# Kernel tuning notes

Hardware: AMD Instinct MI355X
Metric: run time of the kernel (lower is better)

The kernel has to match this reference:

```python
import jax, jax.numpy as jnp
import numpy as np

B, NVEC, DIM, HEADS, DH, M, ITERS, DEPTH, NCLASS, KER = 8, 4096, 512, 8, 64, 256, 6, 2, 10, 33
INNER = HEADS * DH


def _ln(x, g, b, eps=1e-5):
    mu = x.mean(-1, keepdims=True)
    var = ((x - mu) ** 2).mean(-1, keepdims=True)
    return (x - mu) * jax.lax.rsqrt(var + eps) * g + b


def _mp_pinv(x, iters=ITERS):
    # Moore-Penrose pseudo-inverse via Newton-Schulz iterations (lucidrains).
    # x: [b, h, m, m]
    abs_x = jnp.abs(x)
    col = abs_x.sum(-1).max(-1)  # [b, h]
    row = abs_x.sum(-2).max(-1)  # [b, h]
    z = jnp.swapaxes(x, -1, -2) / (col * row)[..., None, None]
    I = jnp.eye(x.shape[-1], dtype=x.dtype)
    for _ in range(iters):
        xz = x @ z
        z = 0.25 * z @ (13.0 * I - xz @ (15.0 * I - xz @ (7.0 * I - xz)))
    return z


def _nystrom_attn(x, qkv_w, out_w, out_b, conv_w):
    b, n, _ = x.shape
    qkv = x @ qkv_w  # [b, n, 3*inner]
    q, k, v = jnp.split(qkv, 3, axis=-1)
    to_h = lambda t: t.reshape(b, n, HEADS, DH).transpose(0, 2, 1, 3)  # [b,h,n,dh]
    q, k, v = to_h(q), to_h(k), to_h(v)
    q = q * (DH ** -0.5)

    l = n // M  # tokens per landmark segment (n divisible by M)
    q_l = q.reshape(b, HEADS, M, l, DH).mean(3)  # [b,h,M,dh]
    k_l = k.reshape(b, HEADS, M, l, DH).mean(3)

    attn1 = jax.nn.softmax(jnp.einsum('bhnd,bhmd->bhnm', q, k_l), axis=-1)    # [b,h,n,M]
    attn2 = jax.nn.softmax(jnp.einsum('bhmd,bhld->bhml', q_l, k_l), axis=-1)  # [b,h,M,M]
    attn3 = jax.nn.softmax(jnp.einsum('bhmd,bhnd->bhmn', q_l, k), axis=-1)    # [b,h,M,n]

    out = (attn1 @ _mp_pinv(attn2)) @ (attn3 @ v)  # [b,h,n,dh]

    # residual depthwise conv over sequence dim (kernel 33, groups=heads, no bias)
    out = out + jax.lax.conv_general_dilated(
        v, conv_w, (1, 1), [(KER // 2, KER // 2), (0, 0)],
        dimension_numbers=('NCHW', 'OIHW', 'NCHW'), feature_group_count=HEADS)

    out = out.transpose(0, 2, 1, 3).reshape(b, n, INNER)
    return out @ out_w + out_b


def setup_inputs():
    key = jax.random.key(0)
    ks = jax.random.split(key, 12)
    s = 0.02
    f32 = jnp.float32
    return {
        'x': jax.random.normal(ks[0], (B, NVEC, 2), f32),
        'lin_w': jax.random.normal(ks[1], (2, DIM), f32) * s,
        'lin_b': jnp.zeros((DIM,), f32),
        'ln1_g': jnp.ones((DEPTH, DIM), f32),
        'ln1_b': jnp.zeros((DEPTH, DIM), f32),
        'qkv_w': jax.random.normal(ks[2], (DEPTH, DIM, 3 * INNER), f32) * s,
        'out_w': jax.random.normal(ks[3], (DEPTH, INNER, DIM), f32) * s,
        'out_b': jnp.zeros((DEPTH, DIM), f32),
        'conv_w': jax.random.normal(ks[4], (DEPTH, HEADS, 1, KER, 1), f32) * s,
        'ln2_g': jnp.ones((DEPTH, DIM), f32),
        'ln2_b': jnp.zeros((DEPTH, DIM), f32),
        'ff1_w': jax.random.normal(ks[5], (DEPTH, DIM, 4 * DIM), f32) * s,
        'ff1_b': jnp.zeros((DEPTH, 4 * DIM), f32),
        'ff2_w': jax.random.normal(ks[6], (DEPTH, 4 * DIM, DIM), f32) * s,
        'ff2_b': jnp.zeros((DEPTH, DIM), f32),
        'final_w': jax.random.normal(ks[7], (NVEC * DIM, NCLASS), f32) * s,
        'final_b': jnp.zeros((NCLASS,), f32),
    }


def reference(x, lin_w, lin_b, ln1_g, ln1_b, qkv_w, out_w, out_b, conv_w,
              ln2_g, ln2_b, ff1_w, ff1_b, ff2_w, ff2_b, final_w, final_b):
    h = x @ lin_w + lin_b  # [B, NVEC, DIM]
    for i in range(DEPTH):
        h = h + _nystrom_attn(_ln(h, ln1_g[i], ln1_b[i]), qkv_w[i], out_w[i], out_b[i], conv_w[i])
        z = _ln(h, ln2_g[i], ln2_b[i])
        h = h + (jax.nn.gelu(z @ ff1_w[i] + ff1_b[i]) @ ff2_w[i] + ff2_b[i])
    return h.reshape(h.shape[0], -1) @ final_w + final_b  # [B, NCLASS]
```

## Files before the change

kernel.cpp:

```cpp
#include <hip/hip_runtime.h>
#include <hip/hip_bf16.h>

#define BB_ 8
#define NVEC 4096
#define DIM 512
#define HEADS 8
#define DH 64
#define MM_ 256
#define ITERS 6
#define DEPTH 2
#define NCLASS 10
#define KER 33
#define INNER 512
#define LSEG 16

typedef long long ll;
typedef __bf16 bh16;
typedef __attribute__((ext_vector_type(8))) __bf16 bf16x8;
typedef __attribute__((ext_vector_type(4))) float f32x4;

template<int WR, int WC, bool TRB, bool GELU_ACT, bool RESID, bool BF16OUT, bool DUAL>
__global__ void __launch_bounds__(256)
mgemm_k(const bh16* __restrict__ A, const bh16* __restrict__ B,
        const float* __restrict__ bias, void* __restrict__ Cv, void* __restrict__ C2v,
        int K, int lda, int ldb, int ldc,
        int BI, ll sAo, ll sAi, ll sBo, ll sBi, ll sCo, ll sCi,
        float alpha, float diagv)
{
    constexpr int BM = WR * 64, BN = WC * 64;
    const int bz = blockIdx.z;
    const int bo = bz / BI, bi = bz % BI;
    const bh16* Ab = A + bo * sAo + (ll)bi * sAi;
    const bh16* Bb = B + bo * sBo + (ll)bi * sBi;
    const ll coff = bo * sCo + (ll)bi * sCi;
    const int m0 = blockIdx.y * BM;
    const int n0 = blockIdx.x * BN;
    const int tid = threadIdx.x;
    const int lane = tid & 63;
    const int wave = tid >> 6;
    const int wr = wave / WC, wc = wave % WC;

    __shared__ bh16 Al[BM * 32];
    __shared__ bh16 Bl[BN * 32];

    f32x4 acc[4][4];
#pragma unroll
    for (int i = 0; i < 4; ++i)
#pragma unroll
        for (int j = 0; j < 4; ++j) acc[i][j] = (f32x4){0.f, 0.f, 0.f, 0.f};

    const int srow = tid >> 2;
    const int ssl  = tid & 3;

    const int rsel  = ((lane & 15) >> 1) & 3;
    const int kslot = lane >> 4;

    for (int k0 = 0; k0 < K; k0 += 32) {
        __syncthreads();
#pragma unroll
        for (int i = 0; i < BM / 64; ++i) {
            int row = i * 64 + srow;
            int gsl = ssl ^ ((row >> 1) & 3);
            __builtin_amdgcn_global_load_lds(
                (const __attribute__((address_space(1))) unsigned int*)
                    (Ab + (ll)(m0 + row) * lda + k0 + gsl * 8),
                (__attribute__((address_space(3))) unsigned int*)
                    (Al + row * 32 + ssl * 8),
                16, 0, 0);
        }
        if (!TRB) {
#pragma unroll
            for (int i = 0; i < BN / 64; ++i) {
                int row = i * 64 + srow;
                int gsl = ssl ^ ((row >> 1) & 3);
                __builtin_amdgcn_global_load_lds(
                    (const __attribute__((address_space(1))) unsigned int*)
                        (Bb + (ll)(n0 + row) * ldb + k0 + gsl * 8),
                    (__attribute__((address_space(3))) unsigned int*)
                        (Bl + row * 32 + ssl * 8),
                    16, 0, 0);
            }
        } else {
            const int bk = tid >> 3;
            const int nb0 = (tid & 7) * (BN / 8);
#pragma unroll
            for (int v8 = 0; v8 < BN / 64; ++v8) {
                int nb = nb0 + v8 * 8;
                bf16x8 v = *(const bf16x8*)(Bb + (ll)(k0 + bk) * ldb + n0 + nb);
#pragma unroll
                for (int j = 0; j < 8; ++j) {
                    int n = nb + j;
                    int sl = (bk >> 3) ^ ((n >> 1) & 3);
                    Bl[n * 32 + sl * 8 + (bk & 7)] = v[j];
                }
            }
        }
        __syncthreads();

        bf16x8 af[4], bfr[4];
#pragma unroll
        for (int mi = 0; mi < 4; ++mi) {
            int row = wr * 64 + mi * 16 + (lane & 15);
            af[mi] = *(const bf16x8*)(Al + row * 32 + (kslot ^ rsel) * 8);
        }
#pragma unroll
        for (int ni = 0; ni < 4; ++ni) {
            int row = wc * 64 + ni * 16 + (lane & 15);
            bfr[ni] = *(const bf16x8*)(Bl + row * 32 + (kslot ^ rsel) * 8);
        }
#pragma unroll
        for (int mi = 0; mi < 4; ++mi)
#pragma unroll
            for (int ni = 0; ni < 4; ++ni)
                acc[mi][ni] = __builtin_amdgcn_mfma_f32_16x16x32_bf16(
                    af[mi], bfr[ni], acc[mi][ni], 0, 0, 0);
    }

#pragma unroll
    for (int mi = 0; mi < 4; ++mi) {
#pragma unroll
        for (int ni = 0; ni < 4; ++ni) {
            const int colg = n0 + wc * 64 + ni * 16 + (lane & 15);
            const float bia = (!DUAL && bias) ? bias[colg] : 0.f;
#pragma unroll
            for (int r = 0; r < 4; ++r) {
                const int rowg = m0 + wr * 64 + mi * 16 + (lane >> 4) * 4 + r;
                const float a = acc[mi][ni][r];
                const ll off = coff + (ll)rowg * ldc + colg;
                if (DUAL) {
                    ((bh16*)Cv)[off] = (bh16)a;
                    float w = ((rowg == colg) ? diagv : 0.f) - a;
                    ((bh16*)C2v)[off] = (bh16)w;
                } else {
                    float v = alpha * a + bia;
                    if (diagv != 0.f && rowg == colg) v += diagv;
                    if (GELU_ACT) {
                        float t = tanhf(0.7978845608f * (v + 0.044715f * v * v * v));
                        v = 0.5f * v * (1.0f + t);
                    }
                    if (BF16OUT) {
                        ((bh16*)Cv)[off] = (bh16)v;
                    } else {
                        float* p = (float*)Cv + off;
                        float o = v;
                        if (RESID) o += *p;
                        *p = o;
                    }
                }
            }
        }
    }
}

template<int WR, int WC, bool TRB, bool G, bool R, bool BO, bool D>
static inline void mg(hipStream_t s, int M, int N, int K,
                      const bh16* A, int lda, const bh16* B, int ldb,
                      void* C, int ldc, void* C2, const float* bias,
                      int batch, int BI,
                      ll sAo, ll sAi, ll sBo, ll sBi, ll sCo, ll sCi,
                      float alpha, float diagv)
{
    dim3 grid(N / (WC * 64), M / (WR * 64), batch);
    hipLaunchKernelGGL((mgemm_k<WR, WC, TRB, G, R, BO, D>), grid, dim3(256), 0, s,
                       A, B, bias, C, C2, K, lda, ldb, ldc, BI,
                       sAo, sAi, sBo, sBi, sCo, sCi, alpha, diagv);
}

__global__ void embed_k(const float* __restrict__ x, const float* __restrict__ w,
                        const float* __restrict__ b, float* __restrict__ h)
{
    ll idx = (ll)blockIdx.x * 256 + threadIdx.x;
    int d = (int)(idx & 511);
    ll bn = idx >> 9;
    h[idx] = x[bn * 2] * w[d] + x[bn * 2 + 1] * w[512 + d] + b[d];
}

__global__ void __launch_bounds__(256)
ln_k(const float* __restrict__ X, const float* __restrict__ g,
     const float* __restrict__ bta, bh16* __restrict__ Y)
{
    const ll row = blockIdx.x;
    const float* x = X + row * 512;
    bh16* y = Y + row * 512;
    const int tid = threadIdx.x;
    float v0 = x[tid], v1 = x[tid + 256];
    float s = v0 + v1;
    float q = v0 * v0 + v1 * v1;
    __shared__ float sred[8];
    for (int o = 32; o; o >>= 1) { s += __shfl_down(s, o); q += __shfl_down(q, o); }
    const int lane = tid & 63, w = tid >> 6;
    if (lane == 0) { sred[w] = s; sred[4 + w] = q; }
    __syncthreads();
    float ssum = sred[0] + sred[1] + sred[2] + sred[3];
    float qsum = sred[4] + sred[5] + sred[6] + sred[7];
    float mu = ssum * (1.0f / 512.0f);
    float var = qsum * (1.0f / 512.0f) - mu * mu;
    float r = rsqrtf(var + 1e-5f);
    y[tid] = (bh16)((v0 - mu) * r * g[tid] + bta[tid]);
    y[tid + 256] = (bh16)((v1 - mu) * r * g[tid + 256] + bta[tid + 256]);
}

__global__ void __launch_bounds__(256)
cvtT_k(const float* __restrict__ in, bh16* __restrict__ outp, int C, int R)
{
    __shared__ float t[64][65];
    const int nCt = C >> 6;
    const int c0 = (blockIdx.x % nCt) * 64;
    const int r0 = (blockIdx.x / nCt) * 64;
    const int tid = threadIdx.x;
#pragma unroll
    for (int j = 0; j < 16; ++j) {
        int idx = j * 256 + tid;
        int lr = idx >> 6, lc = idx & 63;
        t[lc][lr] = in[(ll)(r0 + lr) * C + c0 + lc];
    }
    __syncthreads();
#pragma unroll
    for (int v = 0; v < 2; ++v) {
        int flat = v * 256 + tid;
        int lc = flat >> 3, r8 = (flat & 7) * 8;
        bf16x8 o;
#pragma unroll
        for (int j = 0; j < 8; ++j) o[j] = (bh16)t[lc][r8 + j];
        *(bf16x8*)(outp + (ll)(c0 + lc) * R + r0 + r8) = o;
    }
}

__global__ void landmarks_k(const bh16* __restrict__ qkv,
                            bh16* __restrict__ qlb, bh16* __restrict__ klb)
{
    int idx = blockIdx.x * 256 + threadIdx.x;
    int d = idx & 63;
    int m = (idx >> 6) & 255;
    int h = (idx >> 14) & 7;
    int b = idx >> 17;
    const bh16* base = qkv + (ll)b * (NVEC * 1536) + (ll)(m * LSEG) * 1536 + h * 64 + d;
    float sq = 0.f, sk = 0.f;
#pragma unroll
    for (int l = 0; l < LSEG; ++l) {
        sq += (float)base[(ll)l * 1536];
        sk += (float)base[(ll)l * 1536 + 512];
    }
    ll o = (ll)(b * 8 + h) * 16384 + m * 64 + d;
    qlb[o] = (bh16)(sq * (0.0625f * 0.125f));
    klb[o] = (bh16)(sk * 0.0625f);
}

__global__ void wbt_k(const bh16* __restrict__ wb, bh16* __restrict__ wbt)
{
    int idx = blockIdx.x * 256 + threadIdx.x;
    int d = idx & 63, kg = (idx >> 6) & 31, bhh = idx >> 11;
    const bh16* p = wb + (ll)bhh * 16384 + kg * 8 * 64 + d;
    bf16x8 o;
#pragma unroll
    for (int j = 0; j < 8; ++j) o[j] = p[j * 64];
    *(bf16x8*)(wbt + (ll)bhh * 16384 + d * 256 + kg * 8) = o;
}

__global__ void a3vred_k(const float* __restrict__ part, bh16* __restrict__ outp)
{
    int idx = blockIdx.x * 256 + threadIdx.x;
    int smp = idx >> 17;
    int rest = idx & 131071;
    int h = rest >> 14, o = rest & 16383;
    const float* p = part + (ll)smp * 1048576 + (ll)h * 131072 + o;
    float s = 0.f;
#pragma unroll
    for (int j = 0; j < 8; ++j) s += p[j * 16384];
    outp[(ll)(smp * 8 + h) * 16384 + o] = (bh16)s;
}

__global__ void __launch_bounds__(256)
conv_k(const bh16* __restrict__ qkv, const float* __restrict__ cw,
       bh16* __restrict__ convo)
{
    int idx = blockIdx.x * 256 + threadIdx.x;
    int c8 = idx & 63;
    int ng = (idx >> 6) & 1023;
    int b  = idx >> 16;
    const int n0 = ng * 4;
    const int h = c8 >> 3;
    const bh16* v = qkv + (ll)b * (NVEC * 1536) + 1024 + c8 * 8;

    float wreg[KER];
#pragma unroll
    for (int k = 0; k < KER; ++k) wreg[k] = cw[h * KER + k];

    float acc[4][8];
#pragma unroll
    for (int t = 0; t < 4; ++t)
#pragma unroll
        for (int e = 0; e < 8; ++e) acc[t][e] = 0.f;

#pragma unroll
    for (int m = 0; m < 36; ++m) {
        int nn = n0 + m - (KER / 2);
        bf16x8 vv = {};
        if ((unsigned)nn < (unsigned)NVEC)
            vv = *(const bf16x8*)(v + (ll)nn * 1536);
#pragma unroll
        for (int t = 0; t < 4; ++t) {
            constexpr int KMAX = KER - 1;
            int k = m - t;
            if (k >= 0 && k <= KMAX) {
                float wk = wreg[k];
#pragma unroll
                for (int e = 0; e < 8; ++e)
                    acc[t][e] = fmaf((float)vv[e], wk, acc[t][e]);
            }
        }
    }

    bh16* o = convo + (ll)b * (NVEC * 512) + (ll)n0 * 512 + c8 * 8;
#pragma unroll
    for (int t = 0; t < 4; ++t) {
        bf16x8 ov;
#pragma unroll
        for (int e = 0; e < 8; ++e) ov[e] = (bh16)acc[t][e];
        *(bf16x8*)(o + (ll)t * 512) = ov;
    }
}

__device__ __forceinline__ float blkmax(float m, float* red, int tid)
{
#pragma unroll
    for (int o = 32; o; o >>= 1) m = fmaxf(m, __shfl_down(m, o));
    if ((tid & 63) == 0) red[tid >> 6] = m;
    __syncthreads();
    m = fmaxf(fmaxf(red[0], red[1]), fmaxf(red[2], red[3]));
    __syncthreads();
    return m;
}
__device__ __forceinline__ float blksum(float s, float* red, int tid)
{
#pragma unroll
    for (int o = 32; o; o >>= 1) s += __shfl_down(s, o);
    if ((tid & 63) == 0) red[tid >> 6] = s;
    __syncthreads();
    s = red[0] + red[1] + red[2] + red[3];
    __syncthreads();
    return s;
}

__global__ void __launch_bounds__(256)
softmax_bf_k(bh16* __restrict__ X, int L)
{
    const ll row = blockIdx.x;
    bh16* x = X + row * (ll)L;
    const int tid = threadIdx.x;
    __shared__ float red[4];
    float v[16];
    bf16x8 a = *(const bf16x8*)(x + tid * 8);
    bf16x8 b = *(const bf16x8*)(x + 2048 + tid * 8);
#pragma unroll
    for (int j = 0; j < 8; ++j) { v[j] = (float)a[j]; v[8 + j] = (float)b[j]; }
    float m = -1e30f;
#pragma unroll
    for (int j = 0; j < 16; ++j) m = fmaxf(m, v[j]);
    m = blkmax(m, red, tid);
    float s = 0.f;
#pragma unroll
    for (int j = 0; j < 16; ++j) { v[j] = __expf(v[j] - m); s += v[j]; }
    s = blksum(s, red, tid);
    float inv = 1.0f / s;
    bf16x8 oa, ob;
#pragma unroll
    for (int j = 0; j < 8; ++j) { oa[j] = (bh16)(v[j] * inv); ob[j] = (bh16)(v[8 + j] * inv); }
    *(bf16x8*)(x + tid * 8) = oa;
    *(bf16x8*)(x + 2048 + tid * 8) = ob;
}

__global__ void __launch_bounds__(256)
softmax256_k(bh16* __restrict__ X)
{
    const int tid = threadIdx.x;
    const ll row = (ll)blockIdx.x * 8 + (tid >> 5);
    const int l = tid & 31;
    bh16* x = X + row * 256 + l * 8;
    bf16x8 a = *(const bf16x8*)x;
    float v[8];
#pragma unroll
    for (int j = 0; j < 8; ++j) v[j] = (float)a[j];
    float m = -1e30f;
#pragma unroll
    for (int j = 0; j < 8; ++j) m = fmaxf(m, v[j]);
#pragma unroll
    for (int o = 16; o; o >>= 1) m = fmaxf(m, __shfl_xor(m, o, 32));
    float s = 0.f;
#pragma unroll
    for (int j = 0; j < 8; ++j) { v[j] = __expf(v[j] - m); s += v[j]; }
#pragma unroll
    for (int o = 16; o; o >>= 1) s += __shfl_xor(s, o, 32);
    float inv = 1.0f / s;
    bf16x8 ov;
#pragma unroll
    for (int j = 0; j < 8; ++j) ov[j] = (bh16)(v[j] * inv);
    *(bf16x8*)x = ov;
}

__global__ void __launch_bounds__(256)
pinv_init_k(const bh16* __restrict__ X, bh16* __restrict__ Z)
{
    const ll bh = blockIdx.x;
    const bh16* x = X + bh * 65536;
    bh16* z = Z + bh * 65536;
    const int tid = threadIdx.x;
    float rs = 0.f, cs = 0.f;
    for (int j = 0; j < 256; ++j) {
        rs += fabsf((float)x[tid * 256 + j]);
        cs += fabsf((float)x[j * 256 + tid]);
    }
    __shared__ float rbuf[256], cbuf[256];
    rbuf[tid] = rs; cbuf[tid] = cs;
    __syncthreads();
    for (int o = 128; o; o >>= 1) {
        if (tid < o) {
            rbuf[tid] = fmaxf(rbuf[tid], rbuf[tid + o]);
            cbuf[tid] = fmaxf(cbuf[tid], cbuf[tid + o]);
        }
        __syncthreads();
    }
    float inv = 1.0f / (rbuf[0] * cbuf[0]);
    for (int e = tid; e < 65536; e += 256) {
        int i = e >> 8, j = e & 255;
        z[e] = (bh16)((float)x[j * 256 + i] * inv);
    }
}

__global__ void final_init_k(const float* __restrict__ fb, float* __restrict__ out)
{
    int i = threadIdx.x;
    if (i < BB_ * NCLASS) out[i] = fb[i % NCLASS];
}

__global__ void __launch_bounds__(256)
final_gemv_k(const float* __restrict__ hbuf, const float* __restrict__ w,
             float* __restrict__ out)
{
    const int half = blockIdx.y;
    const int chunk = blockIdx.x;
    const int tid = threadIdx.x;
    const int k0 = chunk * 8192;
    float pc[4][NCLASS] = {};
    for (int e = 0; e < 32; ++e) {
        int k = k0 + e * 256 + tid;
        const float* wr = w + (ll)k * NCLASS;
        float wv[NCLASS];
#pragma unroll
        for (int c = 0; c < NCLASS; ++c) wv[c] = wr[c];
#pragma unroll
        for (int b = 0; b < 4; ++b) {
            float hv = hbuf[(ll)(half * 4 + b) * (NVEC * DIM) + k];
#pragma unroll
            for (int c = 0; c < NCLASS; ++c) pc[b][c] = fmaf(hv, wv[c], pc[b][c]);
        }
    }
    __shared__ float red[4][4][NCLASS];
    const int lane = tid & 63, wv_ = tid >> 6;
#pragma unroll
    for (int b = 0; b < 4; ++b)
#pragma unroll
        for (int c = 0; c < NCLASS; ++c) {
            float s = pc[b][c];
#pragma unroll
            for (int o = 32; o; o >>= 1) s += __shfl_down(s, o);
            if (lane == 0) red[wv_][b][c] = s;
        }
    __syncthreads();
    if (tid < 4 * NCLASS) {
        int b = tid / NCLASS, c = tid % NCLASS;
        float s = red[0][b][c] + red[1][b][c] + red[2][b][c] + red[3][b][c];
        atomicAdd(out + (half * 4 + b) * NCLASS + c, s);
    }
}

extern "C" void kernel_launch(void* const* d_in, const int* in_sizes, int n_in,
                              void* d_out, int out_size, void* d_ws, size_t ws_size,
                              hipStream_t stream)
{
    const float* x      = (const float*)d_in[0];
    const float* lin_w  = (const float*)d_in[1];
    const float* lin_b  = (const float*)d_in[2];
    const float* ln1_g  = (const float*)d_in[3];
    const float* ln1_b  = (const float*)d_in[4];
    const float* qkv_w  = (const float*)d_in[5];
    const float* out_w  = (const float*)d_in[6];
    const float* out_b  = (const float*)d_in[7];
    const float* conv_w = (const float*)d_in[8];
    const float* ln2_g  = (const float*)d_in[9];
    const float* ln2_b  = (const float*)d_in[10];
    const float* ff1_w  = (const float*)d_in[11];
    const float* ff1_b  = (const float*)d_in[12];
    const float* ff2_w  = (const float*)d_in[13];
    const float* ff2_b  = (const float*)d_in[14];
    const float* final_w = (const float*)d_in[15];
    const float* final_b = (const float*)d_in[16];
    float* out = (float*)d_out;
    float* ws  = (float*)d_ws;

    float* H    = ws;
    bh16*  QKV  = (bh16*)(ws + 16777216);
    float* P    = ws + 41943040;
    bh16*  qlbf = (bh16*)(ws + 52428800);
    bh16*  klbf = (bh16*)(ws + 52953088);
    bh16*  A3Vb = (bh16*)(ws + 53477376);
    bh16*  WBb  = (bh16*)(ws + 54001664);
    bh16*  WBT  = (bh16*)(ws + 54525952);
    bh16*  WQT  = (bh16*)(ws + 55050240);
    bh16*  WOT  = (bh16*)(ws + 55443456);
    bh16*  F1WT = (bh16*)(ws + 55574528);
    bh16*  F2WT = (bh16*)(ws + 56098816);
    if (ws_size < 56623104ULL * 4) return;

    bh16*  XLNall = (bh16*)P;
    bh16*  ATT3c  = (bh16*)P;
    float* A3Vp   = P + 8388608;
    bh16*  CONVa  = (bh16*)P;
    bh16*  Xbf = (bh16*)P;
    bh16*  Z0  = (bh16*)(P + 2097152);
    bh16*  Z1  = (bh16*)(P + 4194304);
    bh16*  T1  = (bh16*)(P + 6291456);
    bh16*  T2  = (bh16*)(P + 8388608);
    bh16*  ATT1c  = (bh16*)P;
    bh16*  AOUTc  = (bh16*)(P + 8388608);
    bh16*  XLNc   = (bh16*)P;
    bh16*  HIDc   = (bh16*)(P + 2097152);

    const ll SMP = (ll)NVEC * 1536;

    hipLaunchKernelGGL(embed_k, dim3(65536), dim3(256), 0, stream, x, lin_w, lin_b, H);

    for (int i = 0; i < DEPTH; ++i) {
        const float* wq  = qkv_w + (ll)i * 512 * 1536;
        const float* wo  = out_w + (ll)i * 512 * 512;
        const float* bo  = out_b + (ll)i * 512;
        const float* cw  = conv_w + (ll)i * HEADS * KER;
        const float* g1  = ln1_g + (ll)i * 512;
        const float* b1  = ln1_b + (ll)i * 512;
        const float* g2  = ln2_g + (ll)i * 512;
        const float* b2  = ln2_b + (ll)i * 512;
        const float* f1w = ff1_w + (ll)i * 512 * 2048;
        const float* f1b = ff1_b + (ll)i * 2048;
        const float* f2w = ff2_w + (ll)i * 2048 * 512;
        const float* f2b = ff2_b + (ll)i * 512;

        hipLaunchKernelGGL(cvtT_k, dim3(192), dim3(256), 0, stream, wq, WQT, 1536, 512);
        hipLaunchKernelGGL(cvtT_k, dim3(64), dim3(256), 0, stream, wo, WOT, 512, 512);
        hipLaunchKernelGGL(cvtT_k, dim3(256), dim3(256), 0, stream, f1w, F1WT, 2048, 512);
        hipLaunchKernelGGL(cvtT_k, dim3(256), dim3(256), 0, stream, f2w, F2WT, 512, 2048);

        hipLaunchKernelGGL(ln_k, dim3(32768), dim3(256), 0, stream, H, g1, b1, XLNall);
        mg<2,2,0,0,0,1,0>(stream, 32768, 1536, 512, XLNall, 512, WQT, 512,
            QKV, 1536, nullptr, nullptr, 1, 1, 0,0, 0,0, 0,0, 1.f, 0.f);

        hipLaunchKernelGGL(landmarks_k, dim3(4096), dim3(256), 0, stream, QKV, qlbf, klbf);

        for (int c = 0; c < 4; ++c) {
            const bh16* qkvc = QKV + (ll)c * 2 * SMP;
            mg<2,2,0,0,0,1,0>(stream, 256, 4096, 64,
                qlbf + (ll)c * 262144, 64, qkvc + 512, 1536,
                ATT3c, 4096, nullptr, nullptr, 16, 8,
                131072, 16384, SMP, 64, 8388608LL, 1048576, 1.f, 0.f);
            hipLaunchKernelGGL(softmax_bf_k, dim3(4096), dim3(256), 0, stream, ATT3c, 4096);
            for (int s = 0; s < 2; ++s) {
                mg<4,1,1,0,0,0,0>(stream, 256, 64, 512,
                    ATT3c + (ll)s * 8 * 1048576, 4096, qkvc + (ll)s * SMP + 1024, 1536,
                    A3Vp + (ll)s * 1048576, 64, nullptr, nullptr, 64, 8,
                    1048576, 512, 64, 512LL * 1536, 131072, 16384, 1.f, 0.f);
            }
            hipLaunchKernelGGL(a3vred_k, dim3(1024), dim3(256), 0, stream,
                               A3Vp, A3Vb + (ll)c * 2 * 131072);
        }

        hipLaunchKernelGGL(conv_k, dim3(2048), dim3(256), 0, stream, QKV, cw, CONVa);
        mg<2,2,0,0,1,0,0>(stream, 32768, 512, 512, CONVa, 512, WOT, 512,
            H, 512, nullptr, nullptr, 1, 1, 0,0, 0,0, 0,0, 1.f, 0.f);

        mg<2,2,0,0,0,1,0>(stream, 256, 256, 64, qlbf, 64, klbf, 64,
            Xbf, 256, nullptr, nullptr, 64, 64, 0, 16384, 0, 16384, 0, 65536, 1.f, 0.f);
        hipLaunchKernelGGL(softmax256_k, dim3(2048), dim3(256), 0, stream, Xbf);
        hipLaunchKernelGGL(pinv_init_k, dim3(64), dim3(256), 0, stream, Xbf, Z0);
        bh16* zc = Z0; bh16* zn = Z1;
        for (int it = 0; it < ITERS; ++it) {
            mg<2,2,1,0,0,1,1>(stream, 256, 256, 256, Xbf, 256, zc, 256,
                T1, 256, T2, nullptr, 64, 64, 0, 65536, 0, 65536, 0, 65536, 1.f, 7.f);
            mg<2,2,1,0,0,1,0>(stream, 256, 256, 256, T1, 256, T2, 256,
                zn, 256, nullptr, nullptr, 64, 64, 0, 65536, 0, 65536, 0, 65536, -1.f, 15.f);
            mg<2,2,1,0,0,1,0>(stream, 256, 256, 256, T1, 256, zn, 256,
                T2, 256, nullptr, nullptr, 64, 64, 0, 65536, 0, 65536, 0, 65536, -1.f, 13.f);
            mg<2,2,1,0,0,1,0>(stream, 256, 256, 256, zc, 256, T2, 256,
                zn, 256, nullptr, nullptr, 64, 64, 0, 65536, 0, 65536, 0, 65536, 0.25f, 0.f);
            bh16* t = zc; zc = zn; zn = t;
        }
        mg<4,1,1,0,0,1,0>(stream, 256, 64, 256, zc, 256, A3Vb, 64,
            WBb, 64, nullptr, nullptr, 64, 64, 0, 65536, 0, 16384, 0, 16384, 1.f, 0.f);
        hipLaunchKernelGGL(wbt_k, dim3(512), dim3(256), 0, stream, WBb, WBT);

        for (int c = 0; c < 4; ++c) {
            const bh16* qkvc = QKV + (ll)c * 2 * SMP;
            mg<2,2,0,0,0,1,0>(stream, 4096, 256, 64,
                qkvc, 1536, klbf + (ll)c * 262144, 64,
                ATT1c, 256, nullptr, nullptr, 16, 8,
                SMP, 64, 131072, 16384, 8388608LL, 1048576, 0.125f, 0.f);
            hipLaunchKernelGGL(softmax256_k, dim3(8192), dim3(256), 0, stream, ATT1c);
            mg<4,1,0,0,0,1,0>(stream, 4096, 64, 256,
                ATT1c, 256, WBT + (ll)c * 262144, 256,
                AOUTc, 512, nullptr, nullptr, 16, 8,
                8388608LL, 1048576, 131072, 16384, 2097152LL, 64, 1.f, 0.f);
            mg<2,2,0,0,1,0,0>(stream, 8192, 512, 512, AOUTc, 512, WOT, 512,
                H + (ll)c * 2 * 2097152, 512, nullptr, bo, 1, 1, 0,0, 0,0, 0,0, 1.f, 0.f);
        }

        for (int c = 0; c < 4; ++c) {
            float* Hc = H + (ll)c * 2 * 2097152;
            hipLaunchKernelGGL(ln_k, dim3(8192), dim3(256), 0, stream, Hc, g2, b2, XLNc);
            mg<2,2,0,1,0,1,0>(stream, 8192, 2048, 512, XLNc, 512, F1WT, 512,
                HIDc, 2048, nullptr, f1b, 1, 1, 0,0, 0,0, 0,0, 1.f, 0.f);
            mg<2,2,0,0,1,0,0>(stream, 8192, 512, 2048, HIDc, 2048, F2WT, 2048,
                Hc, 512, nullptr, f2b, 1, 1, 0,0, 0,0, 0,0, 1.f, 0.f);
        }
    }

    hipLaunchKernelGGL(final_init_k, dim3(1), dim3(128), 0, stream, final_b, out);
    hipLaunchKernelGGL(final_gemv_k, dim3(256, 2), dim3(256), 0, stream, H, final_w, out);
}
```

Baseline: 3.526 ms.

## Fuse softmax into GEMM epilogue, fold conv into attention output, remap XCDs

Adds an SMAX epilogue to the GEMM that does a row softmax across the 256-wide tile, using shuffles and LDS for the cross-wave reduction. The separate softmax256 passes over attn1 and attn2 are removed. The depthwise conv output is now written in place over the k slice of QKV and added in the attn1·W GEMM epilogue (ADDC), which drops the extra full out-projection GEMM over the conv output. Workgroups are also remapped so that consecutive tiles land on the same XCD, aiming for better L2 locality. The trade-offs are more registers and syncs in the softmax path and overwriting k, which must no longer be needed by that point.

```diff
diff --git a/kernel.cpp b/kernel.cpp
--- a/kernel.cpp
+++ b/kernel.cpp
@@ -19,12 +19,14 @@
 typedef __attribute__((ext_vector_type(8))) __bf16 bf16x8;
 typedef __attribute__((ext_vector_type(4))) float f32x4;
 
-template<int WR, int WC, bool TRB, bool GELU_ACT, bool RESID, bool BF16OUT, bool DUAL>
+template<int WR, int WC, bool TRB, bool GELU_ACT, bool RESID, bool BF16OUT,
+         bool DUAL, bool SMAX, bool ADDC>
 __global__ void __launch_bounds__(256)
 mgemm_k(const bh16* __restrict__ A, const bh16* __restrict__ B,
         const float* __restrict__ bias, void* __restrict__ Cv, void* __restrict__ C2v,
         int K, int lda, int ldb, int ldc,
         int BI, ll sAo, ll sAi, ll sBo, ll sBi, ll sCo, ll sCi,
+        int ldc2, ll sC2o, ll sC2i,
         float alpha, float diagv)
 {
     constexpr int BM = WR * 64, BN = WC * 64;
@@ -33,8 +35,18 @@
     const bh16* Ab = A + bo * sAo + (ll)bi * sAi;
     const bh16* Bb = B + bo * sBo + (ll)bi * sBi;
     const ll coff = bo * sCo + (ll)bi * sCi;
-    const int m0 = blockIdx.y * BM;
-    const int n0 = blockIdx.x * BN;
+
+    const int gx = gridDim.x;
+    const int nwg = gx * gridDim.y;
+    int flat = blockIdx.y * gx + blockIdx.x;
+    {
+        int xcd = flat & 7, base = flat >> 3;
+        int q = nwg >> 3, rr = nwg & 7;
+        flat = (xcd < rr ? xcd * (q + 1) : rr * (q + 1) + (xcd - rr) * q) + base;
+    }
+    const int m0 = (flat / gx) * BM;
+    const int n0 = (flat % gx) * BN;
+
     const int tid = threadIdx.x;
     const int lane = tid & 63;
     const int wave = tid >> 6;
@@ -42,6 +54,7 @@
 
     __shared__ bh16 Al[BM * 32];
     __shared__ bh16 Bl[BN * 32];
+    __shared__ float srow[SMAX ? 4 * 64 : 4];
 
     f32x4 acc[4][4];
 #pragma unroll
@@ -49,8 +62,8 @@
 #pragma unroll
         for (int j = 0; j < 4; ++j) acc[i][j] = (f32x4){0.f, 0.f, 0.f, 0.f};
 
-    const int srow = tid >> 2;
-    const int ssl  = tid & 3;
+    const int srowi = tid >> 2;
+    const int ssl   = tid & 3;
 
     const int rsel  = ((lane & 15) >> 1) & 3;
     const int kslot = lane >> 4;
@@ -59,7 +72,7 @@
         __syncthreads();
 #pragma unroll
         for (int i = 0; i < BM / 64; ++i) {
-            int row = i * 64 + srow;
+            int row = i * 64 + srowi;
             int gsl = ssl ^ ((row >> 1) & 3);
             __builtin_amdgcn_global_load_lds(
                 (const __attribute__((address_space(1))) unsigned int*)
@@ -71,7 +84,7 @@
         if (!TRB) {
 #pragma unroll
             for (int i = 0; i < BN / 64; ++i) {
-                int row = i * 64 + srow;
+                int row = i * 64 + srowi;
                 int gsl = ssl ^ ((row >> 1) & 3);
                 __builtin_amdgcn_global_load_lds(
                     (const __attribute__((address_space(1))) unsigned int*)
@@ -116,6 +129,88 @@
                     af[mi], bfr[ni], acc[mi][ni], 0, 0, 0);
     }
 
+    if (SMAX) {
+        bh16* Cb = (bh16*)Cv;
+#pragma unroll
+        for (int mi = 0; mi < 4; ++mi)
+#pragma unroll
+            for (int ni = 0; ni < 4; ++ni)
+#pragma unroll
+                for (int r = 0; r < 4; ++r) acc[mi][ni][r] *= alpha;
+        float mx[4][4];
+#pragma unroll
+        for (int mi = 0; mi < 4; ++mi)
+#pragma unroll
+            for (int r = 0; r < 4; ++r) {
+                float m_ = acc[mi][0][r];
+#pragma unroll
+                for (int ni = 1; ni < 4; ++ni) m_ = fmaxf(m_, acc[mi][ni][r]);
+#pragma unroll
+                for (int msk = 1; msk < 16; msk <<= 1)
+                    m_ = fmaxf(m_, __shfl_xor(m_, msk));
+                mx[mi][r] = m_;
+            }
+        if ((lane & 15) == 0) {
+#pragma unroll
+            for (int mi = 0; mi < 4; ++mi)
+#pragma unroll
+                for (int r = 0; r < 4; ++r)
+                    srow[wc * 64 + mi * 16 + (lane >> 4) * 4 + r] = mx[mi][r];
+        }
+        __syncthreads();
+        float M_[4][4];
+#pragma unroll
+        for (int mi = 0; mi < 4; ++mi)
+#pragma unroll
+            for (int r = 0; r < 4; ++r) {
+                int row = mi * 16 + (lane >> 4) * 4 + r;
+                M_[mi][r] = fmaxf(fmaxf(srow[row], srow[64 + row]),
+                                  fmaxf(srow[128 + row], srow[192 + row]));
+            }
+        __syncthreads();
+        float sm[4][4];
+#pragma unroll
+        for (int mi = 0; mi < 4; ++mi)
+#pragma unroll
+            for (int r = 0; r < 4; ++r) {
+                float s_ = 0.f;
+#pragma unroll
+                for (int ni = 0; ni < 4; ++ni) {
+                    float e = __expf(acc[mi][ni][r] - M_[mi][r]);
+                    acc[mi][ni][r] = e;
+                    s_ += e;
+                }
+#pragma unroll
+                for (int msk = 1; msk < 16; msk <<= 1)
+                    s_ += __shfl_xor(s_, msk);
+                sm[mi][r] = s_;
+            }
+        if ((lane & 15) == 0) {
+#pragma unroll
+            for (int mi = 0; mi < 4; ++mi)
+#pragma unroll
+                for (int r = 0; r < 4; ++r)
+                    srow[wc * 64 + mi * 16 + (lane >> 4) * 4 + r] = sm[mi][r];
+        }
+        __syncthreads();
+#pragma unroll
+        for (int mi = 0; mi < 4; ++mi)
+#pragma unroll
+            for (int r = 0; r < 4; ++r) {
+                int row = mi * 16 + (lane >> 4) * 4 + r;
+                float inv = 1.0f / (srow[row] + srow[64 + row] +
+                                    srow[128 + row] + srow[192 + row]);
+                int rowg = m0 + row;
+#pragma unroll
+                for (int ni = 0; ni < 4; ++ni) {
+                    int colg = n0 + wc * 64 + ni * 16 + (lane & 15);
+                    Cb[coff + (ll)rowg * ldc + colg] = (bh16)(acc[mi][ni][r] * inv);
+                }
+            }
+        return;
+    }
+
+    const ll c2off = ADDC ? (bo * sC2o + (ll)bi * sC2i) : 0;
 #pragma unroll
     for (int mi = 0; mi < 4; ++mi) {
 #pragma unroll
@@ -133,6 +228,8 @@
                     ((bh16*)C2v)[off] = (bh16)w;
                 } else {
                     float v = alpha * a + bia;
+                    if (ADDC)
+                        v += (float)((const bh16*)C2v)[c2off + (ll)rowg * ldc2 + colg];
                     if (diagv != 0.f && rowg == colg) v += diagv;
                     if (GELU_ACT) {
                         float t = tanhf(0.7978845608f * (v + 0.044715f * v * v * v));
@@ -152,18 +249,19 @@
     }
 }
 
-template<int WR, int WC, bool TRB, bool G, bool R, bool BO, bool D>
+template<int WR, int WC, bool TRB, bool G, bool R, bool BO, bool D, bool SX, bool AC>
 static inline void mg(hipStream_t s, int M, int N, int K,
                       const bh16* A, int lda, const bh16* B, int ldb,
                       void* C, int ldc, void* C2, const float* bias,
                       int batch, int BI,
                       ll sAo, ll sAi, ll sBo, ll sBi, ll sCo, ll sCi,
-                      float alpha, float diagv)
+                      float alpha, float diagv,
+                      int ldc2 = 0, ll sC2o = 0, ll sC2i = 0)
 {
     dim3 grid(N / (WC * 64), M / (WR * 64), batch);
-    hipLaunchKernelGGL((mgemm_k<WR, WC, TRB, G, R, BO, D>), grid, dim3(256), 0, s,
+    hipLaunchKernelGGL((mgemm_k<WR, WC, TRB, G, R, BO, D, SX, AC>), grid, dim3(256), 0, s,
                        A, B, bias, C, C2, K, lda, ldb, ldc, BI,
-                       sAo, sAi, sBo, sBi, sCo, sCi, alpha, diagv);
+                       sAo, sAi, sBo, sBi, sCo, sCi, ldc2, sC2o, sC2i, alpha, diagv);
 }
 
 __global__ void embed_k(const float* __restrict__ x, const float* __restrict__ w,
@@ -271,8 +369,7 @@
 }
 
 __global__ void __launch_bounds__(256)
-conv_k(const bh16* __restrict__ qkv, const float* __restrict__ cw,
-       bh16* __restrict__ convo)
+conv_k(bh16* __restrict__ qkv, const float* __restrict__ cw)
 {
     int idx = blockIdx.x * 256 + threadIdx.x;
     int c8 = idx & 63;
@@ -311,13 +408,13 @@
         }
     }
 
-    bh16* o = convo + (ll)b * (NVEC * 512) + (ll)n0 * 512 + c8 * 8;
+    bh16* o = qkv + (ll)b * (NVEC * 1536) + (ll)n0 * 1536 + 512 + c8 * 8;
 #pragma unroll
     for (int t = 0; t < 4; ++t) {
         bf16x8 ov;
 #pragma unroll
         for (int e = 0; e < 8; ++e) ov[e] = (bh16)acc[t][e];
-        *(bf16x8*)(o + (ll)t * 512) = ov;
+        *(bf16x8*)(o + (ll)t * 1536) = ov;
     }
 }
 
@@ -368,34 +465,6 @@
     for (int j = 0; j < 8; ++j) { oa[j] = (bh16)(v[j] * inv); ob[j] = (bh16)(v[8 + j] * inv); }
     *(bf16x8*)(x + tid * 8) = oa;
     *(bf16x8*)(x + 2048 + tid * 8) = ob;
-}
-
-__global__ void __launch_bounds__(256)
-softmax256_k(bh16* __restrict__ X)
-{
-    const int tid = threadIdx.x;
-    const ll row = (ll)blockIdx.x * 8 + (tid >> 5);
-    const int l = tid & 31;
-    bh16* x = X + row * 256 + l * 8;
-    bf16x8 a = *(const bf16x8*)x;
-    float v[8];
-#pragma unroll
-    for (int j = 0; j < 8; ++j) v[j] = (float)a[j];
-    float m = -1e30f;
-#pragma unroll
-    for (int j = 0; j < 8; ++j) m = fmaxf(m, v[j]);
-#pragma unroll
-    for (int o = 16; o; o >>= 1) m = fmaxf(m, __shfl_xor(m, o, 32));
-    float s = 0.f;
-#pragma unroll
-    for (int j = 0; j < 8; ++j) { v[j] = __expf(v[j] - m); s += v[j]; }
-#pragma unroll
-    for (int o = 16; o; o >>= 1) s += __shfl_xor(s, o, 32);
-    float inv = 1.0f / s;
-    bf16x8 ov;
-#pragma unroll
-    for (int j = 0; j < 8; ++j) ov[j] = (bh16)(v[j] * inv);
-    *(bf16x8*)x = ov;
 }
 
 __global__ void __launch_bounds__(256)
@@ -515,7 +584,6 @@
     bh16*  XLNall = (bh16*)P;
     bh16*  ATT3c  = (bh16*)P;
     float* A3Vp   = P + 8388608;
-    bh16*  CONVa  = (bh16*)P;
     bh16*  Xbf = (bh16*)P;
     bh16*  Z0  = (bh16*)(P + 2097152);
     bh16*  Z1  = (bh16*)(P + 4194304);
@@ -550,20 +618,20 @@
         hipLaunchKernelGGL(cvtT_k, dim3(256), dim3(256), 0, stream, f2w, F2WT, 512, 2048);
 
         hipLaunchKernelGGL(ln_k, dim3(32768), dim3(256), 0, stream, H, g1, b1, XLNall);
-        mg<2,2,0,0,0,1,0>(stream, 32768, 1536, 512, XLNall, 512, WQT, 512,
+        mg<2,2,0,0,0,1,0,0,0>(stream, 32768, 1536, 512, XLNall, 512, WQT, 512,
             QKV, 1536, nullptr, nullptr, 1, 1, 0,0, 0,0, 0,0, 1.f, 0.f);
 
         hipLaunchKernelGGL(landmarks_k, dim3(4096), dim3(256), 0, stream, QKV, qlbf, klbf);
 
         for (int c = 0; c < 4; ++c) {
             const bh16* qkvc = QKV + (ll)c * 2 * SMP;
-            mg<2,2,0,0,0,1,0>(stream, 256, 4096, 64,
+            mg<2,2,0,0,0,1,0,0,0>(stream, 256, 4096, 64,
                 qlbf + (ll)c * 262144, 64, qkvc + 512, 1536,
                 ATT3c, 4096, nullptr, nullptr, 16, 8,
                 131072, 16384, SMP, 64, 8388608LL, 1048576, 1.f, 0.f);
             hipLaunchKernelGGL(softmax_bf_k, dim3(4096), dim3(256), 0, stream, ATT3c, 4096);
             for (int s = 0; s < 2; ++s) {
-                mg<4,1,1,0,0,0,0>(stream, 256, 64, 512,
+                mg<4,1,1,0,0,0,0,0,0>(stream, 256, 64, 512,
                     ATT3c + (ll)s * 8 * 1048576, 4096, qkvc + (ll)s * SMP + 1024, 1536,
                     A3Vp + (ll)s * 1048576, 64, nullptr, nullptr, 64, 8,
                     1048576, 512, 64, 512LL * 1536, 131072, 16384, 1.f, 0.f);
@@ -572,51 +640,49 @@
                                A3Vp, A3Vb + (ll)c * 2 * 131072);
         }
 
-        hipLaunchKernelGGL(conv_k, dim3(2048), dim3(256), 0, stream, QKV, cw, CONVa);
-        mg<2,2,0,0,1,0,0>(stream, 32768, 512, 512, CONVa, 512, WOT, 512,
-            H, 512, nullptr, nullptr, 1, 1, 0,0, 0,0, 0,0, 1.f, 0.f);
-
-        mg<2,2,0,0,0,1,0>(stream, 256, 256, 64, qlbf, 64, klbf, 64,
+        hipLaunchKernelGGL(conv_k, dim3(2048), dim3(256), 0, stream, QKV, cw);
+
+        mg<1,4,0,0,0,1,0,1,0>(stream, 256, 256, 64, qlbf, 64, klbf, 64,
             Xbf, 256, nullptr, nullptr, 64, 64, 0, 16384, 0, 16384, 0, 65536, 1.f, 0.f);
-        hipLaunchKernelGGL(softmax256_k, dim3(2048), dim3(256), 0, stream, Xbf);
         hipLaunchKernelGGL(pinv_init_k, dim3(64), dim3(256), 0, stream, Xbf, Z0);
         bh16* zc = Z0; bh16* zn = Z1;
         for (int it = 0; it < ITERS; ++it) {
-            mg<2,2,1,0,0,1,1>(stream, 256, 256, 256, Xbf, 256, zc, 256,
-                T1, 256, T2, nullptr, 64, 64, 0, 65536, 0, 65536, 0, 65536, 1.f, 7.f);
-            mg<2,2,1,0,0,1,0>(stream, 256, 256, 256, T1, 256, T2, 256,
+            mg<2,2,1,0,0,1,1,0,0>(stream, 256, 256, 256, Xbf, 256, zc, 256,
+                T1, 256, T2, nullptr, 64, 64, 0, 65536, 0, 65536, 0, 65536, 1.f, 7.f,
+                256, 0, 65536);
+            mg<2,2,1,0,0,1,0,0,0>(stream, 256, 256, 256, T1, 256, T2, 256,
                 zn, 256, nullptr, nullptr, 64, 64, 0, 65536, 0, 65536, 0, 65536, -1.f, 15.f);
-            mg<2,2,1,0,0,1,0>(stream, 256, 256, 256, T1, 256, zn, 256,
+            mg<2,2,1,0,0,1,0,0,0>(stream, 256, 256, 256, T1, 256, zn, 256,
                 T2, 256, nullptr, nullptr, 64, 64, 0, 65536, 0, 65536, 0, 65536, -1.f, 13.f);
-            mg<2,2,1,0,0,1,0>(stream, 256, 256, 256, zc, 256, T2, 256,
+            mg<2,2,1,0,0,1,0,0,0>(stream, 256, 256, 256, zc, 256, T2, 256,
                 zn, 256, nullptr, nullptr, 64, 64, 0, 65536, 0, 65536, 0, 65536, 0.25f, 0.f);
             bh16* t = zc; zc = zn; zn = t;
         }
-        mg<4,1,1,0,0,1,0>(stream, 256, 64, 256, zc, 256, A3Vb, 64,
+        mg<4,1,1,0,0,1,0,0,0>(stream, 256, 64, 256, zc, 256, A3Vb, 64,
             WBb, 64, nullptr, nullptr, 64, 64, 0, 65536, 0, 16384, 0, 16384, 1.f, 0.f);
         hipLaunchKernelGGL(wbt_k, dim3(512), dim3(256), 0, stream, WBb, WBT);
 
         for (int c = 0; c < 4; ++c) {
             const bh16* qkvc = QKV + (ll)c * 2 * SMP;
-            mg<2,2,0,0,0,1,0>(stream, 4096, 256, 64,
+            mg<1,4,0,0,0,1,0,1,0>(stream, 4096, 256, 64,
                 qkvc, 1536, klbf + (ll)c * 262144, 64,
                 ATT1c, 256, nullptr, nullptr, 16, 8,
                 SMP, 64, 131072, 16384, 8388608LL, 1048576, 0.125f, 0.f);
-            hipLaunchKernelGGL(softmax256_k, dim3(8192), dim3(256), 0, stream, ATT1c);
-            mg<4,1,0,0,0,1,0>(stream, 4096, 64, 256,
+            mg<4,1,0,0,0,1,0,0,1>(stream, 4096, 64, 256,
                 ATT1c, 256, WBT + (ll)c * 262144, 256,
-                AOUTc, 512, nullptr, nullptr, 16, 8,
-                8388608LL, 1048576, 131072, 16384, 2097152LL, 64, 1.f, 0.f);
-            mg<2,2,0,0,1,0,0>(stream, 8192, 512, 512, AOUTc, 512, WOT, 512,
+                AOUTc, 512, (void*)(QKV + (ll)c * 2 * SMP + 512), nullptr, 16, 8,
+                8388608LL, 1048576, 131072, 16384, 2097152LL, 64, 1.f, 0.f,
+                1536, SMP, 64);
+            mg<2,2,0,0,1,0,0,0,0>(stream, 8192, 512, 512, AOUTc, 512, WOT, 512,
                 H + (ll)c * 2 * 2097152, 512, nullptr, bo, 1, 1, 0,0, 0,0, 0,0, 1.f, 0.f);
         }
 
         for (int c = 0; c < 4; ++c) {
             float* Hc = H + (ll)c * 2 * 2097152;
             hipLaunchKernelGGL(ln_k, dim3(8192), dim3(256), 0, stream, Hc, g2, b2, XLNc);
-            mg<2,2,0,1,0,1,0>(stream, 8192, 2048, 512, XLNc, 512, F1WT, 512,
+            mg<2,2,0,1,0,1,0,0,0>(stream, 8192, 2048, 512, XLNc, 512, F1WT, 512,
                 HIDc, 2048, nullptr, f1b, 1, 1, 0,0, 0,0, 0,0, 1.f, 0.f);
-            mg<2,2,0,0,1,0,0>(stream, 8192, 512, 2048, HIDc, 2048, F2WT, 2048,
+            mg<2,2,0,0,1,0,0,0,0>(stream, 8192, 512, 2048, HIDc, 2048, F2WT, 2048,
                 Hc, 512, nullptr, f2b, 1, 1, 0,0, 0,0, 0,0, 1.f, 0.f);
         }
     }
```

New measurement: 3.388 ms. 1.04x faster.
